# Kernel tuning notes

Measured on AMD Instinct MI355X. Metric: run time of the kernel, lower is better.

Reference implementation:

```python
import jax, jax.numpy as jnp
import numpy as np

T, B, I, H = 256, 128, 1024, 1024


def setup_inputs() -> dict:
    key = jax.random.key(0)
    ks = jax.random.split(key, 5)
    # weight init ranges per LSTMLayer.__init__ with wb=0 (no quantization):
    lim_hh = 1.0 / np.sqrt(H)
    lim_ih = 1.0 / np.sqrt(I)
    return {
        "x": jax.random.normal(ks[0], (T, B, I), dtype=jnp.float32),
        "h0": jax.random.normal(ks[1], (B, H), dtype=jnp.float32),
        "c0": jax.random.normal(ks[2], (B, H), dtype=jnp.float32),
        "W_ih": jax.random.uniform(ks[3], (4 * H, I), dtype=jnp.float32, minval=-lim_ih, maxval=lim_ih),
        "W_hh": jax.random.uniform(ks[4], (4 * H, H), dtype=jnp.float32, minval=-lim_hh, maxval=lim_hh),
        "b_ih": jnp.zeros((4 * H,), dtype=jnp.float32),   # uniform_(0, 0)
        "b_hh": jnp.ones((4 * H,), dtype=jnp.float32),    # uniform_(1, 1)
    }


def reference(x, h0, c0, W_ih, W_hh, b_ih, b_hh):
    # Standard LSTM cell, rolled over time with lax.scan.
    # gates layout follows torch LSTMCell: [i, f, g, o] chunks of size H.
    Wih_T = W_ih.T  # [I, 4H]
    Whh_T = W_hh.T  # [H, 4H]
    bias = b_ih + b_hh  # [4H]

    def step(carry, xt):
        h, c = carry  # [B,H] each
        gates = xt @ Wih_T + h @ Whh_T + bias  # [B, 4H]
        i, f, g, o = jnp.split(gates, 4, axis=-1)
        i = jax.nn.sigmoid(i)
        f = jax.nn.sigmoid(f)
        g = jnp.tanh(g)
        o = jax.nn.sigmoid(o)
        c_new = f * c + i * g
        h_new = o * jnp.tanh(c_new)
        return (h_new, c_new), h_new

    (hT, cT), ys = jax.lax.scan(step, (h0, c0), x)
    return ys, hT, cT  # ys: [T, B, H]
```

## Files before the change

### kernel.cpp

```cpp
#include <hip/hip_runtime.h>

#define T_ 256
#define B_ 128
#define I_ 1024
#define H_ 1024
#define G_ 4096
#define BH (B_*H_)
#define TB (T_*B_)

typedef float f32x4 __attribute__((ext_vector_type(4)));
typedef short bf16x8 __attribute__((ext_vector_type(8)));

__device__ inline unsigned short f2bf(float f) {
    union { float f; unsigned int u; } v; v.f = f;
    unsigned int u = v.u;
    unsigned int r = (u + 0x7fffu + ((u >> 16) & 1u)) >> 16;
    return (unsigned short)r;
}
__device__ inline float bf2f(unsigned short s) {
    union { unsigned int u; float f; } v; v.u = ((unsigned int)s) << 16;
    return v.f;
}
__device__ inline float sigmoidf_(float x) { return 1.0f / (1.0f + __expf(-x)); }
__device__ inline float tanhf_(float x) {
    x = fminf(15.0f, fmaxf(-15.0f, x));
    float e = __expf(2.0f * x);
    return (e - 1.0f) / (e + 1.0f);
}

__global__ void cvt_kernel(const float* __restrict__ src, unsigned short* __restrict__ dst, int n) {
    int i = (blockIdx.x * blockDim.x + threadIdx.x) * 4;
    int stride = gridDim.x * blockDim.x * 4;
    for (; i < n; i += stride) {
        float4 v = *reinterpret_cast<const float4*>(src + i);
        ushort4 o;
        o.x = f2bf(v.x); o.y = f2bf(v.y); o.z = f2bf(v.z); o.w = f2bf(v.w);
        *reinterpret_cast<ushort4*>(dst + i) = o;
    }
}

__global__ void bias_kernel(const float* __restrict__ a, const float* __restrict__ b, float* __restrict__ out) {
    int i = blockIdx.x * blockDim.x + threadIdx.x;
    if (i < G_) out[i] = a[i] + b[i];
}

__global__ __launch_bounds__(256) void pregemm(
    const unsigned short* __restrict__ xb,
    const unsigned short* __restrict__ wih,
    const float* __restrict__ bias,
    unsigned short* __restrict__ gx)
{
    int wgid = (blockIdx.x & 7) * 1024 + (blockIdx.x >> 3);
    int mg = wgid & 255;
    int ng = wgid >> 8;
    int m0 = mg * 128, n0 = ng * 128;
    int tid = threadIdx.x;
    int w = tid >> 6, l = tid & 63;
    int qm = (w >> 1) * 64, qn = (w & 1) * 64;
    int lr = l & 15, lk = (l >> 4) * 8, lq = l >> 4;

    const unsigned short* ap = xb  + (size_t)(m0 + qm + lr) * I_ + lk;
    const unsigned short* bp = wih + (size_t)(n0 + qn + lr) * I_ + lk;

    f32x4 acc[4][4] = {};
    #pragma unroll 4
    for (int kk = 0; kk < 32; ++kk) {
        bf16x8 a[4], b[4];
        #pragma unroll
        for (int mt = 0; mt < 4; ++mt)
            a[mt] = *reinterpret_cast<const bf16x8*>(ap + (size_t)mt * 16 * I_ + kk * 32);
        #pragma unroll
        for (int nt = 0; nt < 4; ++nt)
            b[nt] = *reinterpret_cast<const bf16x8*>(bp + (size_t)nt * 16 * I_ + kk * 32);
        #pragma unroll
        for (int mt = 0; mt < 4; ++mt)
            #pragma unroll
            for (int nt = 0; nt < 4; ++nt)
                acc[mt][nt] = __builtin_amdgcn_mfma_f32_16x16x32_bf16(a[mt], b[nt], acc[mt][nt], 0, 0, 0);
    }
    #pragma unroll
    for (int mt = 0; mt < 4; ++mt) {
        #pragma unroll
        for (int nt = 0; nt < 4; ++nt) {
            #pragma unroll
            for (int r = 0; r < 4; ++r) {
                int m = m0 + qm + mt * 16 + lq * 4 + r;
                int n = n0 + qn + nt * 16 + lr;
                gx[(size_t)m * G_ + n] = f2bf(acc[mt][nt][r] + bias[n]);
            }
        }
    }
}

__global__ __launch_bounds__(256) void lstm_step(
    const unsigned short* __restrict__ hprev,
    const unsigned short* __restrict__ whh,
    const unsigned short* __restrict__ gxt,
    float* __restrict__ c,
    float* __restrict__ yst,
    unsigned short* __restrict__ hnext)
{
    __shared__ float lds_g[4][32][16];
    int mg = blockIdx.x >> 6;
    int ng = blockIdx.x & 63;
    int tid = threadIdx.x;
    int w = tid >> 6, l = tid & 63;
    int lr = l & 15, lk = (l >> 4) * 8, lq = l >> 4;
    int m0 = mg * 32, n0 = ng * 16;

    const unsigned short* ap = hprev + (size_t)(m0 + lr) * H_ + lk;
    const unsigned short* bp = whh   + (size_t)(w * 1024 + n0 + lr) * H_ + lk;

    f32x4 acc0 = {}, acc1 = {};
    #pragma unroll 8
    for (int kk = 0; kk < 32; ++kk) {
        bf16x8 a0 = *reinterpret_cast<const bf16x8*>(ap + kk * 32);
        bf16x8 a1 = *reinterpret_cast<const bf16x8*>(ap + (size_t)16 * H_ + kk * 32);
        bf16x8 bb = *reinterpret_cast<const bf16x8*>(bp + kk * 32);
        acc0 = __builtin_amdgcn_mfma_f32_16x16x32_bf16(a0, bb, acc0, 0, 0, 0);
        acc1 = __builtin_amdgcn_mfma_f32_16x16x32_bf16(a1, bb, acc1, 0, 0, 0);
    }
    #pragma unroll
    for (int r = 0; r < 4; ++r) {
        lds_g[w][lq * 4 + r][lr]      = acc0[r];
        lds_g[w][16 + lq * 4 + r][lr] = acc1[r];
    }
    __syncthreads();

    #pragma unroll
    for (int e = 0; e < 2; ++e) {
        int idx = tid + e * 256;
        int row = idx >> 4, col = idx & 15;
        size_t gb = (size_t)(m0 + row) * G_ + n0 + col;
        float gi = lds_g[0][row][col] + bf2f(gxt[gb]);
        float gf = lds_g[1][row][col] + bf2f(gxt[gb + 1024]);
        float gg = lds_g[2][row][col] + bf2f(gxt[gb + 2048]);
        float go = lds_g[3][row][col] + bf2f(gxt[gb + 3072]);
        float iv = sigmoidf_(gi);
        float fv = sigmoidf_(gf);
        float gv = tanhf_(gg);
        float ov = sigmoidf_(go);
        size_t ho = (size_t)(m0 + row) * H_ + n0 + col;
        float cn = fv * c[ho] + iv * gv;
        c[ho] = cn;
        float hn = ov * tanhf_(cn);
        yst[ho] = hn;
        hnext[ho] = f2bf(hn);
    }
}

extern "C" void kernel_launch(void* const* d_in, const int* in_sizes, int n_in,
                              void* d_out, int out_size, void* d_ws, size_t ws_size,
                              hipStream_t stream)
{
    const float* x   = (const float*)d_in[0];
    const float* h0  = (const float*)d_in[1];
    const float* c0  = (const float*)d_in[2];
    const float* Wih = (const float*)d_in[3];
    const float* Whh = (const float*)d_in[4];
    const float* bih = (const float*)d_in[5];
    const float* bhh = (const float*)d_in[6];

    char* ws = (char*)d_ws;
    unsigned short* gx   = (unsigned short*)(ws);
    unsigned short* xb   = (unsigned short*)(ws + 268435456);
    unsigned short* wihb = (unsigned short*)(ws + 335544320);
    unsigned short* whhb = (unsigned short*)(ws + 343932928);
    unsigned short* hbuf = (unsigned short*)(ws + 352321536);
    float*          bias = (float*)(ws + 352845824);

    float* out = (float*)d_out;
    float* ys = out;
    float* hT = out + (size_t)TB * H_;
    float* cT = hT + BH;

    cvt_kernel<<<2048, 256, 0, stream>>>(x,   xb,   TB * I_);
    cvt_kernel<<<512,  256, 0, stream>>>(Wih, wihb, G_ * I_);
    cvt_kernel<<<512,  256, 0, stream>>>(Whh, whhb, G_ * H_);
    cvt_kernel<<<128,  256, 0, stream>>>(h0,  hbuf, BH);
    bias_kernel<<<16, 256, 0, stream>>>(bih, bhh, bias);
    hipMemcpyAsync(cT, c0, (size_t)BH * sizeof(float), hipMemcpyDeviceToDevice, stream);

    pregemm<<<8192, 256, 0, stream>>>(xb, wihb, bias, gx);

    for (int t = 0; t < T_; ++t) {
        lstm_step<<<256, 256, 0, stream>>>(
            hbuf + (size_t)(t & 1) * BH,
            whhb,
            gx + (size_t)t * B_ * G_,
            cT,
            ys + (size_t)t * BH,
            hbuf + (size_t)((t + 1) & 1) * BH);
    }
    hipMemcpyAsync(hT, ys + (size_t)(T_ - 1) * BH, (size_t)BH * sizeof(float), hipMemcpyDeviceToDevice, stream);
}
```

Baseline: 4.757 ms.

## Replace per-step launches with persistent recurrent kernel using grid barrier

After: 5.987 ms. 25.9% more time.

```diff
diff --git a/kernel.cpp b/kernel.cpp
--- a/kernel.cpp
+++ b/kernel.cpp
@@ -92,60 +92,95 @@
     }
 }
 
-__global__ __launch_bounds__(256) void lstm_step(
-    const unsigned short* __restrict__ hprev,
+__device__ __forceinline__ void grid_barrier(unsigned* bar, int step, int bid) {
+    __syncthreads();
+    if (threadIdx.x == 0) {
+        __threadfence();
+        unsigned target = (unsigned)(step * 16 + 15);
+        unsigned old = atomicAdd(bar + (bid & 15) * 32, 1u);
+        if (old == target) {
+            unsigned mold = atomicAdd(bar + 512, 1u);
+            if (mold == target) {
+                __hip_atomic_store(bar + 544, (unsigned)(step + 1),
+                                   __ATOMIC_RELEASE, __HIP_MEMORY_SCOPE_AGENT);
+            }
+        }
+        while (__hip_atomic_load(bar + 544, __ATOMIC_RELAXED, __HIP_MEMORY_SCOPE_AGENT)
+               < (unsigned)(step + 1)) {
+            __builtin_amdgcn_s_sleep(2);
+        }
+        __threadfence();
+    }
+    __syncthreads();
+}
+
+__global__ __launch_bounds__(512) void lstm_recur(
     const unsigned short* __restrict__ whh,
-    const unsigned short* __restrict__ gxt,
-    float* __restrict__ c,
-    float* __restrict__ yst,
-    unsigned short* __restrict__ hnext)
+    const unsigned short* __restrict__ gx,
+    const float* __restrict__ c0,
+    unsigned short* __restrict__ hbuf,
+    float* __restrict__ ys,
+    float* __restrict__ hT, float* __restrict__ cT,
+    unsigned* __restrict__ bar)
 {
-    __shared__ float lds_g[4][32][16];
-    int mg = blockIdx.x >> 6;
-    int ng = blockIdx.x & 63;
-    int tid = threadIdx.x;
-    int w = tid >> 6, l = tid & 63;
-    int lr = l & 15, lk = (l >> 4) * 8, lq = l >> 4;
-    int m0 = mg * 32, n0 = ng * 16;
-
-    const unsigned short* ap = hprev + (size_t)(m0 + lr) * H_ + lk;
-    const unsigned short* bp = whh   + (size_t)(w * 1024 + n0 + lr) * H_ + lk;
-
-    f32x4 acc0 = {}, acc1 = {};
-    #pragma unroll 8
-    for (int kk = 0; kk < 32; ++kk) {
-        bf16x8 a0 = *reinterpret_cast<const bf16x8*>(ap + kk * 32);
-        bf16x8 a1 = *reinterpret_cast<const bf16x8*>(ap + (size_t)16 * H_ + kk * 32);
-        bf16x8 bb = *reinterpret_cast<const bf16x8*>(bp + kk * 32);
-        acc0 = __builtin_amdgcn_mfma_f32_16x16x32_bf16(a0, bb, acc0, 0, 0, 0);
-        acc1 = __builtin_amdgcn_mfma_f32_16x16x32_bf16(a1, bb, acc1, 0, 0, 0);
-    }
-    #pragma unroll
-    for (int r = 0; r < 4; ++r) {
-        lds_g[w][lq * 4 + r][lr]      = acc0[r];
-        lds_g[w][16 + lq * 4 + r][lr] = acc1[r];
-    }
-    __syncthreads();
-
-    #pragma unroll
-    for (int e = 0; e < 2; ++e) {
-        int idx = tid + e * 256;
-        int row = idx >> 4, col = idx & 15;
-        size_t gb = (size_t)(m0 + row) * G_ + n0 + col;
-        float gi = lds_g[0][row][col] + bf2f(gxt[gb]);
-        float gf = lds_g[1][row][col] + bf2f(gxt[gb + 1024]);
-        float gg = lds_g[2][row][col] + bf2f(gxt[gb + 2048]);
-        float go = lds_g[3][row][col] + bf2f(gxt[gb + 3072]);
+    __shared__ float lds_g[2][4][32][16];
+    const int bid = blockIdx.x;
+    const int mg = bid >> 6, ng = bid & 63;
+    const int m0 = mg * 32, n0 = ng * 16;
+    const int tid = threadIdx.x;
+    const int w = tid >> 6, l = tid & 63;
+    const int g = w & 3, kh = w >> 2;
+    const int lr = l & 15, lk8 = (l >> 4) * 8, lq = l >> 4;
+
+    const int erow = tid >> 4, ecol = tid & 15;
+    const size_t eoff = (size_t)(m0 + erow) * H_ + n0 + ecol;
+    float c = c0[eoff];
+    const unsigned short* gxp = gx + (size_t)(m0 + erow) * G_ + n0 + ecol;
+
+    const unsigned short* bp = whh + (size_t)(g * 1024 + n0 + lr) * H_ + kh * 512 + lk8;
+
+    unsigned short gx0 = gxp[0], gx1 = gxp[1024], gx2 = gxp[2048], gx3 = gxp[3072];
+
+    for (int t = 0; t < T_; ++t) {
+        const unsigned short* hp = hbuf + (size_t)(t & 1) * BH
+                                 + (size_t)(m0 + lr) * H_ + kh * 512 + lk8;
+        f32x4 acc0 = {}, acc1 = {};
+        #pragma unroll
+        for (int kk = 0; kk < 16; ++kk) {
+            bf16x8 bb = *reinterpret_cast<const bf16x8*>(bp + kk * 32);
+            bf16x8 a0 = *reinterpret_cast<const bf16x8*>(hp + kk * 32);
+            bf16x8 a1 = *reinterpret_cast<const bf16x8*>(hp + (size_t)16 * H_ + kk * 32);
+            acc0 = __builtin_amdgcn_mfma_f32_16x16x32_bf16(a0, bb, acc0, 0, 0, 0);
+            acc1 = __builtin_amdgcn_mfma_f32_16x16x32_bf16(a1, bb, acc1, 0, 0, 0);
+        }
+        #pragma unroll
+        for (int r = 0; r < 4; ++r) {
+            lds_g[kh][g][lq * 4 + r][lr]      = acc0[r];
+            lds_g[kh][g][16 + lq * 4 + r][lr] = acc1[r];
+        }
+        __syncthreads();
+
+        float gi = lds_g[0][0][erow][ecol] + lds_g[1][0][erow][ecol] + bf2f(gx0);
+        float gf = lds_g[0][1][erow][ecol] + lds_g[1][1][erow][ecol] + bf2f(gx1);
+        float gg = lds_g[0][2][erow][ecol] + lds_g[1][2][erow][ecol] + bf2f(gx2);
+        float go = lds_g[0][3][erow][ecol] + lds_g[1][3][erow][ecol] + bf2f(gx3);
         float iv = sigmoidf_(gi);
         float fv = sigmoidf_(gf);
         float gv = tanhf_(gg);
         float ov = sigmoidf_(go);
-        size_t ho = (size_t)(m0 + row) * H_ + n0 + col;
-        float cn = fv * c[ho] + iv * gv;
-        c[ho] = cn;
-        float hn = ov * tanhf_(cn);
-        yst[ho] = hn;
-        hnext[ho] = f2bf(hn);
+        c = fv * c + iv * gv;
+        float hn = ov * tanhf_(c);
+
+        ys[(size_t)t * BH + eoff] = hn;
+        hbuf[(size_t)((t + 1) & 1) * BH + eoff] = f2bf(hn);
+        if (t == T_ - 1) { hT[eoff] = hn; cT[eoff] = c; }
+
+        if (t + 1 < T_) {
+            const unsigned short* p = gxp + (size_t)(t + 1) * B_ * G_;
+            gx0 = p[0]; gx1 = p[1024]; gx2 = p[2048]; gx3 = p[3072];
+        }
+
+        grid_barrier(bar, t, bid);
     }
 }
 
@@ -168,29 +203,21 @@
     unsigned short* whhb = (unsigned short*)(ws + 343932928);
     unsigned short* hbuf = (unsigned short*)(ws + 352321536);
     float*          bias = (float*)(ws + 352845824);
+    unsigned*       bar  = (unsigned*)(ws + 352862208);
 
     float* out = (float*)d_out;
     float* ys = out;
     float* hT = out + (size_t)TB * H_;
     float* cT = hT + BH;
 
+    hipMemsetAsync(bar, 0, 4096, stream);
     cvt_kernel<<<2048, 256, 0, stream>>>(x,   xb,   TB * I_);
     cvt_kernel<<<512,  256, 0, stream>>>(Wih, wihb, G_ * I_);
     cvt_kernel<<<512,  256, 0, stream>>>(Whh, whhb, G_ * H_);
     cvt_kernel<<<128,  256, 0, stream>>>(h0,  hbuf, BH);
     bias_kernel<<<16, 256, 0, stream>>>(bih, bhh, bias);
-    hipMemcpyAsync(cT, c0, (size_t)BH * sizeof(float), hipMemcpyDeviceToDevice, stream);
 
     pregemm<<<8192, 256, 0, stream>>>(xb, wihb, bias, gx);
 
-    for (int t = 0; t < T_; ++t) {
-        lstm_step<<<256, 256, 0, stream>>>(
-            hbuf + (size_t)(t & 1) * BH,
-            whhb,
-            gx + (size_t)t * B_ * G_,
-            cT,
-            ys + (size_t)t * BH,
-            hbuf + (size_t)((t + 1) & 1) * BH);
-    }
-    hipMemcpyAsync(hT, ys + (size_t)(T_ - 1) * BH, (size_t)BH * sizeof(float), hipMemcpyDeviceToDevice, stream);
-}
+    lstm_recur<<<256, 512, 0, stream>>>(whhb, gx, c0, hbuf, ys, hT, cT, bar);
+}
```
